# Optimization experiments

Measured on AMD Instinct MI355X. Metric: run time of the kernel, lower is better.

## Reference

```python
import jax, jax.numpy as jnp
import numpy as np

SCALE = 500.0  # config.scale
RADIUS = 1.1   # config.radius


def setup_inputs() -> dict:
    key = jax.random.key(0)
    k1, k2, k3 = jax.random.split(key, 3)
    N, D, T, R, B = 65536, 3, 64, 64, 64
    x = jax.random.normal(k1, (N, D), dtype=jnp.float32)
    directions = jax.random.normal(k2, (D, T), dtype=jnp.float32)
    directions = directions / jnp.linalg.norm(directions, axis=0, keepdims=True)  # unit directions
    lin = jnp.linspace(-RADIUS, RADIUS, R, dtype=jnp.float32)
    batch = jnp.sort(jax.random.randint(k3, (N,), 0, B)).astype(jnp.int64)
    return {"x": x, "directions": directions, "lin": lin, "batch": batch, "dim_size": B}


def reference(x, directions, lin, batch, dim_size):
    # nh: height of each point along each direction. [N, T]
    nh = x @ directions
    N, T = nh.shape
    R = lin.shape[0]
    # Sigmoid-smoothed indicator of (height <= threshold). [N, R, T]
    ecc = jax.nn.sigmoid(SCALE * (lin[None, :, None] - nh[:, None, :]))
    # Scatter-accumulate per point cloud. [B, R, T]
    ect = jax.ops.segment_sum(
        ecc.reshape(N, R * T), batch, num_segments=dim_size,
        indices_are_sorted=True,
    ).reshape(dim_size, R, T)
    return ect
```

## Files before the change

kernel.cpp:

```cpp
#include <hip/hip_runtime.h>


#define T_DIRS   64
#define R_STEPS  64
#define NROWS    67
#define ROWW     5
#define N_BATCH  64
#define TSPLIT   16
#define TQW      4
#define PSW      16
#define THREADS  512
#define NWAVES   8
#define SSTRIDE  256
#define MAXSAMP  512

#define RADIUS_F 1.1f
#define STEP_F   (2.0f * RADIUS_F / (R_STEPS - 1))
#define INV_STEP (1.0f / STEP_F)
#define OFF_F    (RADIUS_F * INV_STEP)
#define MEXP     (-500.0f * STEP_F * 1.4426950408889634f)
#define FIXP     16384.0f
#define FIXP_U   16384u
#define INV_FIXP (1.0f / 16384.0f)

__global__ __launch_bounds__(THREADS) void ect_kernel(
    const float* __restrict__ x,
    const float* __restrict__ dirs,
    const int*   __restrict__ batch,
    float* __restrict__ out,
    int N)
{
    __shared__ unsigned s_a[NROWS * ROWW];
    __shared__ unsigned s_ws[NWAVES * TQW];
    __shared__ int      s_samp[MAXSAMP];
    __shared__ int      s_ks_lo, s_ks_hi, s_lo, s_hi;

    const int tid  = threadIdx.x;
    const int b    = blockIdx.x >> 4;
    const int q    = blockIdx.x & (TSPLIT - 1);
    const int lane = tid & 63;
    const int w    = tid >> 6;
    const int ps   = lane >> 2;
    const int tq   = lane & (TQW - 1);
    const int tg   = q * TQW + tq;

    const int nsamp = (N + SSTRIDE - 1) / SSTRIDE;

    for (int i = tid; i < NROWS * ROWW; i += THREADS) s_a[i] = 0u;
    if (tid == 0) { s_ks_lo = nsamp; s_ks_hi = nsamp; s_lo = N; s_hi = N; }
    for (int k = tid; k < nsamp; k += THREADS) s_samp[k] = batch[k * SSTRIDE];

    const float d0 = dirs[tg];
    const float d1 = dirs[T_DIRS + tg];
    const float d2 = dirs[2 * T_DIRS + tg];
    __syncthreads();

    for (int k = tid; k < nsamp; k += THREADS) {
        int v  = s_samp[k];
        int vp = (k == 0) ? -1 : s_samp[k - 1];
        if (v >= b && vp < b)  s_ks_lo = k;
        if (v >  b && vp <= b) s_ks_hi = k;
    }
    __syncthreads();

    if (tid <= SSTRIDE) {
        int kl = s_ks_lo, kh = s_ks_hi;
        int w0 = (kl == 0) ? 0 : (kl - 1) * SSTRIDE;
        int w1 = (kl >= nsamp) ? N : min(N, kl * SSTRIDE + 1);
        int j  = w0 + tid;
        if (j < w1) {
            int v  = batch[j];
            int vp = (j == 0) ? -1 : batch[j - 1];
            if (v >= b && vp < b) s_lo = j;
        }
        int h0 = (kh == 0) ? 0 : (kh - 1) * SSTRIDE;
        int h1 = (kh >= nsamp) ? N : min(N, kh * SSTRIDE + 1);
        j = h0 + tid;
        if (j < h1) {
            int v  = batch[j];
            int vp = (j == 0) ? -1 : batch[j - 1];
            if (v > b && vp <= b) s_hi = j;
        }
    }
    __syncthreads();
    const int lo = s_lo, hi = s_hi;
    const int len = hi - lo;

    for (int p = w * PSW + ps; p < len; p += NWAVES * PSW) {
        int g = lo + p;
        float x0 = x[g * 3 + 0];
        float x1 = x[g * 3 + 1];
        float x2 = x[g * 3 + 2];
        float nh  = fmaf(x2, d2, fmaf(x1, d1, x0 * d0));
        float u   = fmaf(nh, INV_STEP, OFF_F);
        float r0f = rintf(u);
        float dd  = r0f - u;
        float e   = __builtin_amdgcn_exp2f(dd * MEXP);
        float s   = __builtin_amdgcn_rcpf(1.0f + e);
        unsigned si = (unsigned)fmaf(s, FIXP, 0.5f);
        int j1 = min(max((int)r0f + 1, 0), R_STEPS + 1);
        unsigned* cell = &s_a[j1 * ROWW + tq];
        atomicAdd(cell, si);
        atomicAdd(cell + ROWW, FIXP_U - si);
    }
    __syncthreads();

    const int rl = ps & 7;
    unsigned v = s_a[(8 * w + 1 + rl) * ROWW + tq];
    unsigned wsum = v;
    wsum += __shfl_xor(wsum, 4, 64);
    wsum += __shfl_xor(wsum, 8, 64);
    wsum += __shfl_xor(wsum, 16, 64);
    if (lane < TQW) s_ws[w * TQW + tq] = wsum;
    __syncthreads();

    if (ps < 8) {
        unsigned run = s_a[tq];
        for (int w2 = 0; w2 < w; ++w2) run += s_ws[w2 * TQW + tq];
#pragma unroll
        for (int i = 1; i <= 7; ++i)
            if (i <= rl) run += s_a[(8 * w + i) * ROWW + tq];
        run += v;
        int r = 8 * w + rl;
        out[((size_t)b << 12) | (r << 6) | tg] = (float)run * INV_FIXP;
    }
}

extern "C" void kernel_launch(void* const* d_in, const int* in_sizes, int n_in,
                              void* d_out, int out_size, void* d_ws, size_t ws_size,
                              hipStream_t stream) {
    const float* x     = (const float*)d_in[0];
    const float* dirs  = (const float*)d_in[1];
    const int*   batch = (const int*)d_in[3];
    float* out = (float*)d_out;
    const int N = in_sizes[3];

    ect_kernel<<<dim3(N_BATCH * TSPLIT), dim3(THREADS), 0, stream>>>(
        x, dirs, batch, out, N);
}
```

Before: 12.70 us.

## Precompute segment offsets in separate kernel and pack count+weight into one 64-bit atomic

Segment boundaries are now found once by a small offsets kernel that writes per-batch start indices to workspace, replacing the per-block sampled binary search over batch that every one of the 1024 blocks repeated. The histogram kernel packs an integer count (high 32 bits) and fixed-point sigmoid weight (low bits) into a single 64-bit LDS atomic per point instead of two 32-bit atomics. The prefix scan is rebuilt to combine the integer counts with the fractional weight of the next row. This adds a second kernel launch and its launch/dependency latency, and relies on 64-bit LDS atomics being cheap.

```diff
diff --git a/kernel.cpp b/kernel.cpp
--- a/kernel.cpp
+++ b/kernel.cpp
@@ -3,16 +3,13 @@
 
 #define T_DIRS   64
 #define R_STEPS  64
-#define NROWS    67
-#define ROWW     5
+#define NROWS    66
 #define N_BATCH  64
 #define TSPLIT   16
 #define TQW      4
 #define PSW      16
 #define THREADS  512
 #define NWAVES   8
-#define SSTRIDE  256
-#define MAXSAMP  512
 
 #define RADIUS_F 1.1f
 #define STEP_F   (2.0f * RADIUS_F / (R_STEPS - 1))
@@ -20,20 +17,28 @@
 #define OFF_F    (RADIUS_F * INV_STEP)
 #define MEXP     (-500.0f * STEP_F * 1.4426950408889634f)
 #define FIXP     16384.0f
-#define FIXP_U   16384u
 #define INV_FIXP (1.0f / 16384.0f)
 
-__global__ __launch_bounds__(THREADS) void ect_kernel(
+__global__ __launch_bounds__(256) void offsets_kernel(
+    const int* __restrict__ batch, int N, unsigned* __restrict__ off)
+{
+    int i = blockIdx.x * 256 + threadIdx.x;
+    if (i >= N) return;
+    int v  = batch[i];
+    int vp = (i == 0) ? -1 : batch[i - 1];
+    for (int b = vp + 1; b <= v; ++b) off[b] = (unsigned)i;
+    if (i == N - 1)
+        for (int b = v + 1; b <= N_BATCH; ++b) off[b] = (unsigned)N;
+}
+
+__global__ __launch_bounds__(THREADS) void hist_kernel(
     const float* __restrict__ x,
     const float* __restrict__ dirs,
-    const int*   __restrict__ batch,
-    float* __restrict__ out,
-    int N)
+    const unsigned* __restrict__ off,
+    float* __restrict__ out)
 {
-    __shared__ unsigned s_a[NROWS * ROWW];
+    __shared__ unsigned long long s_a[NROWS * TQW];
     __shared__ unsigned s_ws[NWAVES * TQW];
-    __shared__ int      s_samp[MAXSAMP];
-    __shared__ int      s_ks_lo, s_ks_hi, s_lo, s_hi;
 
     const int tid  = threadIdx.x;
     const int b    = blockIdx.x >> 4;
@@ -44,48 +49,17 @@
     const int tq   = lane & (TQW - 1);
     const int tg   = q * TQW + tq;
 
-    const int nsamp = (N + SSTRIDE - 1) / SSTRIDE;
-
-    for (int i = tid; i < NROWS * ROWW; i += THREADS) s_a[i] = 0u;
-    if (tid == 0) { s_ks_lo = nsamp; s_ks_hi = nsamp; s_lo = N; s_hi = N; }
-    for (int k = tid; k < nsamp; k += THREADS) s_samp[k] = batch[k * SSTRIDE];
+    for (int i = tid; i < NROWS * TQW; i += THREADS) s_a[i] = 0ull;
 
     const float d0 = dirs[tg];
     const float d1 = dirs[T_DIRS + tg];
     const float d2 = dirs[2 * T_DIRS + tg];
+
+    const int lo  = (int)off[b];
+    const int len = (int)off[b + 1] - lo;
     __syncthreads();
 
-    for (int k = tid; k < nsamp; k += THREADS) {
-        int v  = s_samp[k];
-        int vp = (k == 0) ? -1 : s_samp[k - 1];
-        if (v >= b && vp < b)  s_ks_lo = k;
-        if (v >  b && vp <= b) s_ks_hi = k;
-    }
-    __syncthreads();
-
-    if (tid <= SSTRIDE) {
-        int kl = s_ks_lo, kh = s_ks_hi;
-        int w0 = (kl == 0) ? 0 : (kl - 1) * SSTRIDE;
-        int w1 = (kl >= nsamp) ? N : min(N, kl * SSTRIDE + 1);
-        int j  = w0 + tid;
-        if (j < w1) {
-            int v  = batch[j];
-            int vp = (j == 0) ? -1 : batch[j - 1];
-            if (v >= b && vp < b) s_lo = j;
-        }
-        int h0 = (kh == 0) ? 0 : (kh - 1) * SSTRIDE;
-        int h1 = (kh >= nsamp) ? N : min(N, kh * SSTRIDE + 1);
-        j = h0 + tid;
-        if (j < h1) {
-            int v  = batch[j];
-            int vp = (j == 0) ? -1 : batch[j - 1];
-            if (v > b && vp <= b) s_hi = j;
-        }
-    }
-    __syncthreads();
-    const int lo = s_lo, hi = s_hi;
-    const int len = hi - lo;
-
+#pragma unroll 2
     for (int p = w * PSW + ps; p < len; p += NWAVES * PSW) {
         int g = lo + p;
         float x0 = x[g * 3 + 0];
@@ -99,15 +73,14 @@
         float s   = __builtin_amdgcn_rcpf(1.0f + e);
         unsigned si = (unsigned)fmaf(s, FIXP, 0.5f);
         int j1 = min(max((int)r0f + 1, 0), R_STEPS + 1);
-        unsigned* cell = &s_a[j1 * ROWW + tq];
-        atomicAdd(cell, si);
-        atomicAdd(cell + ROWW, FIXP_U - si);
+        atomicAdd(&s_a[j1 * TQW + tq],
+                  (1ull << 32) | (unsigned long long)si);
     }
     __syncthreads();
 
     const int rl = ps & 7;
-    unsigned v = s_a[(8 * w + 1 + rl) * ROWW + tq];
-    unsigned wsum = v;
+    unsigned c = (unsigned)(s_a[(8 * w + rl) * TQW + tq] >> 32);
+    unsigned wsum = c;
     wsum += __shfl_xor(wsum, 4, 64);
     wsum += __shfl_xor(wsum, 8, 64);
     wsum += __shfl_xor(wsum, 16, 64);
@@ -115,14 +88,15 @@
     __syncthreads();
 
     if (ps < 8) {
-        unsigned run = s_a[tq];
+        unsigned run = 0;
         for (int w2 = 0; w2 < w; ++w2) run += s_ws[w2 * TQW + tq];
 #pragma unroll
-        for (int i = 1; i <= 7; ++i)
-            if (i <= rl) run += s_a[(8 * w + i) * ROWW + tq];
-        run += v;
+        for (int i = 0; i < 8; ++i)
+            if (i <= rl) run += (unsigned)(s_a[(8 * w + i) * TQW + tq] >> 32);
+        unsigned si = (unsigned)s_a[(8 * w + rl + 1) * TQW + tq];
         int r = 8 * w + rl;
-        out[((size_t)b << 12) | (r << 6) | tg] = (float)run * INV_FIXP;
+        out[((size_t)b << 12) | (r << 6) | tg] =
+            (float)run + (float)si * INV_FIXP;
     }
 }
 
@@ -135,6 +109,8 @@
     float* out = (float*)d_out;
     const int N = in_sizes[3];
 
-    ect_kernel<<<dim3(N_BATCH * TSPLIT), dim3(THREADS), 0, stream>>>(
-        x, dirs, batch, out, N);
+    unsigned* off = (unsigned*)d_ws;
+
+    offsets_kernel<<<dim3((N + 255) / 256), dim3(256), 0, stream>>>(batch, N, off);
+    hist_kernel<<<dim3(N_BATCH * TSPLIT), dim3(THREADS), 0, stream>>>(x, dirs, off, out);
 }
```

Measured after the change: 15.98 us. +25.8%, slower.
